# Optimization experiments

Measured on AMD Instinct MI355X. Metric: run time of the kernel, lower is better.

Reference implementation:

```python
import jax, jax.numpy as jnp
import numpy as np

N_NODES = 50000
N_EDGES = 600000
IN_DIM = 64
HID = 128
LN_EPS = 1e-5


def setup_inputs() -> dict:
    key = jax.random.key(0)
    ks = jax.random.split(key, 10)
    x = jax.random.normal(ks[0], (N_NODES, IN_DIM), dtype=jnp.float32)
    edge_index = jax.random.randint(ks[1], (2, N_EDGES), 0, N_NODES, dtype=jnp.int64)
    def lin(k, fan_in, fan_out):
        bound = 1.0 / np.sqrt(fan_in)
        kw, kb = jax.random.split(k)
        W = jax.random.uniform(kw, (fan_in, fan_out), minval=-bound, maxval=bound, dtype=jnp.float32)
        b = jax.random.uniform(kb, (fan_out,), minval=-bound, maxval=bound, dtype=jnp.float32)
        return W, b
    W1, b1 = lin(ks[2], IN_DIM, HID)
    W2, b2 = lin(ks[3], HID, HID)
    W3, b3 = lin(ks[4], HID, HID)
    g1 = jnp.ones((HID,), jnp.float32); be1 = jnp.zeros((HID,), jnp.float32)
    g2 = jnp.ones((HID,), jnp.float32); be2 = jnp.zeros((HID,), jnp.float32)
    g3 = jnp.ones((HID,), jnp.float32); be3 = jnp.zeros((HID,), jnp.float32)
    return dict(x=x, edge_index=edge_index, W1=W1, b1=b1, W2=W2, b2=b2, W3=W3, b3=b3,
                g1=g1, be1=be1, g2=g2, be2=be2, g3=g3, be3=be3)


def _gnn_layer(h, W, b, src, dst, inv_cnt, g, be):
    # linear transform then mean aggregation over {neighbors ∪ self} (self-loops in src/dst)
    h = h @ W + b                                   # [N, HID]
    s = jax.ops.segment_sum(h[src], dst, num_segments=N_NODES)  # gather + scatter-sum
    h = s * inv_cnt                                 # mean aggregation
    h = jax.nn.relu(h)
    mu = jnp.mean(h, axis=-1, keepdims=True)
    var = jnp.var(h, axis=-1, keepdims=True)
    return g * (h - mu) * jax.lax.rsqrt(var + LN_EPS) + be


def reference(x, edge_index, W1, b1, W2, b2, W3, b3, g1, be1, g2, be2, g3, be3):
    loops = jnp.arange(N_NODES, dtype=edge_index.dtype)
    src = jnp.concatenate([edge_index[0], loops])   # message source (x_j)
    dst = jnp.concatenate([edge_index[1], loops])   # aggregation target
    cnt = jax.ops.segment_sum(jnp.ones_like(dst, dtype=x.dtype), dst, num_segments=N_NODES)
    inv_cnt = (1.0 / cnt)[:, None]                  # cnt >= 1 due to self loops
    h = _gnn_layer(x, W1, b1, src, dst, inv_cnt, g1, be1)
    h = _gnn_layer(h, W2, b2, src, dst, inv_cnt, g2, be2)
    h = _gnn_layer(h, W3, b3, src, dst, inv_cnt, g3, be3)
    return h
```

## Files before the change

### kernel.cpp

```cpp
#include <hip/hip_runtime.h>
#include <hip/hip_bf16.h>

#define N_NODES 50000
#define N_EDGES 600000
#define HID 128
#define LN_EPS 1e-5f

#define SCAN_BLOCK 1024
#define SCAN_NBLK ((N_NODES + SCAN_BLOCK - 1) / SCAN_BLOCK)

typedef __attribute__((ext_vector_type(8))) short bf16x8;
typedef __attribute__((ext_vector_type(4))) float f32x4;

static __device__ __forceinline__ unsigned short f2bf(float f) {
    union { float f; unsigned u; } v; v.f = f;
    unsigned u = v.u;
    u += 0x7fffu + ((u >> 16) & 1u);
    return (unsigned short)(u >> 16);
}
static __device__ __forceinline__ float bflo(unsigned u) {
    union { unsigned u; float f; } c; c.u = u << 16; return c.f;
}
static __device__ __forceinline__ float bfhi(unsigned u) {
    union { unsigned u; float f; } c; c.u = u & 0xffff0000u; return c.f;
}

__global__ __launch_bounds__(256) void count_kernel(const int* __restrict__ ei,
                                                    int* __restrict__ deg, int E) {
    int i = blockIdx.x * blockDim.x + threadIdx.x;
    if (i < E) atomicAdd(&deg[ei[E + i]], 1);
}

__global__ __launch_bounds__(SCAN_BLOCK) void deg_partial_kernel(const int* __restrict__ deg,
                                                                 int* __restrict__ partials, int n) {
    int t = threadIdx.x;
    int i = blockIdx.x * SCAN_BLOCK + t;
    int v = (i < n) ? deg[i] : 0;
    int s = v;
#pragma unroll
    for (int off = 1; off < 64; off <<= 1) s += __shfl_xor(s, off);
    __shared__ int ws[SCAN_BLOCK / 64];
    if ((t & 63) == 0) ws[t >> 6] = s;
    __syncthreads();
    if (t == 0) {
        int tot = 0;
#pragma unroll
        for (int w = 0; w < SCAN_BLOCK / 64; ++w) tot += ws[w];
        partials[blockIdx.x] = tot;
    }
}

__global__ __launch_bounds__(64) void scan_partials_kernel(int* __restrict__ partials,
                                                           int* __restrict__ row_ptr, int nblk) {
    int lane = threadIdx.x;
    int v = (lane < nblk) ? partials[lane] : 0;
    int incl = v;
#pragma unroll
    for (int off = 1; off < 64; off <<= 1) {
        int x = __shfl_up(incl, off);
        if (lane >= off) incl += x;
    }
    if (lane < nblk) partials[lane] = incl - v;
    if (lane == 63) row_ptr[N_NODES] = incl;
}

__global__ __launch_bounds__(SCAN_BLOCK) void scan_final_kernel(const int* __restrict__ deg,
                                                                const int* __restrict__ partials,
                                                                int* __restrict__ row_ptr,
                                                                int* __restrict__ cursor,
                                                                float* __restrict__ inv_cnt, int n) {
    int t = threadIdx.x;
    int i = blockIdx.x * SCAN_BLOCK + t;
    int v = (i < n) ? deg[i] : 0;
    int lane = t & 63, wid = t >> 6;
    int incl = v;
#pragma unroll
    for (int off = 1; off < 64; off <<= 1) {
        int x = __shfl_up(incl, off);
        if (lane >= off) incl += x;
    }
    __shared__ int ws[SCAN_BLOCK / 64];
    if (lane == 63) ws[wid] = incl;
    __syncthreads();
    int woff = 0;
    for (int w = 0; w < wid; ++w) woff += ws[w];
    int excl = partials[blockIdx.x] + woff + (incl - v);
    if (i < n) {
        row_ptr[i] = excl;
        cursor[i]  = excl;
        inv_cnt[i] = 1.0f / (float)(v + 1);
    }
}

__global__ __launch_bounds__(256) void fill_kernel(const int* __restrict__ ei,
                                                   int* __restrict__ cursor,
                                                   int* __restrict__ col, int E) {
    int i = blockIdx.x * blockDim.x + threadIdx.x;
    if (i < E) {
        int s = ei[i];
        int d = ei[E + i];
        int p = atomicAdd(&cursor[d], 1);
        col[p] = s;
    }
}

__global__ __launch_bounds__(256) void cast_x_kernel(const float* __restrict__ x,
                                                     unsigned short* __restrict__ xb, int n8) {
    int i = blockIdx.x * 256 + threadIdx.x;
    if (i < n8) {
        float4 a = ((const float4*)x)[i * 2];
        float4 b = ((const float4*)x)[i * 2 + 1];
        int4 o;
        o.x = (int)f2bf(a.x) | ((int)f2bf(a.y) << 16);
        o.y = (int)f2bf(a.z) | ((int)f2bf(a.w) << 16);
        o.z = (int)f2bf(b.x) | ((int)f2bf(b.y) << 16);
        o.w = (int)f2bf(b.z) | ((int)f2bf(b.w) << 16);
        ((int4*)xb)[i] = o;
    }
}

__global__ __launch_bounds__(256) void wswz_kernel(const float* __restrict__ W,
                                                   unsigned short* __restrict__ dst, int K) {
    int i = blockIdx.x * 256 + threadIdx.x;
    if (i < K * 128) {
        int k = i >> 7, col = i & 127;
        dst[(((k >> 3) * 128) + col) * 8 + (k & 7)] = f2bf(W[i]);
    }
}

template <int K>
__global__ __launch_bounds__(256) void gemm_mfma_kernel(
    const unsigned short* __restrict__ A,
    const unsigned short* __restrict__ Wswz,
    const float* __restrict__ bias,
    unsigned short* __restrict__ out, int N) {
    __shared__ unsigned short Bl[K * 128];
    __shared__ float bl[128];
    int t = threadIdx.x;
    for (int i = t; i < K * 16; i += 256)
        ((int4*)Bl)[i] = ((const int4*)Wswz)[i];
    if (t < 128) bl[t] = bias[t];
    __syncthreads();

    int lane = t & 63;
    int w = t >> 6;
    int r0 = blockIdx.x * 64 + w * 16;
    int colb = lane & 15;
    int kg = lane >> 4;
    int rowa = min(r0 + colb, N - 1);

    f32x4 acc[8];
#pragma unroll
    for (int c = 0; c < 8; ++c) acc[c] = (f32x4){0.f, 0.f, 0.f, 0.f};

    const bf16x8* Blv = (const bf16x8*)Bl;
    for (int s = 0; s < K; s += 32) {
        bf16x8 afrag = *(const bf16x8*)&A[(size_t)rowa * K + s + kg * 8];
        int kb = (s >> 3) + kg;
#pragma unroll
        for (int c = 0; c < 8; ++c) {
            bf16x8 bfrag = Blv[kb * 128 + c * 16 + colb];
            acc[c] = __builtin_amdgcn_mfma_f32_16x16x32_bf16(afrag, bfrag, acc[c], 0, 0, 0);
        }
    }
#pragma unroll
    for (int c = 0; c < 8; ++c) {
        int col = c * 16 + colb;
        float bv = bl[col];
#pragma unroll
        for (int r = 0; r < 4; ++r) {
            int ro = r0 + kg * 4 + r;
            if (ro < N) out[(size_t)ro * 128 + col] = f2bf(acc[c][r] + bv);
        }
    }
}

template <int BF16OUT>
__global__ __launch_bounds__(256) void agg_norm_kernel(
    const unsigned short* __restrict__ hb,
    const int* __restrict__ row_ptr,
    const int* __restrict__ col,
    const float* __restrict__ inv_cnt,
    const float* __restrict__ g, const float* __restrict__ be,
    void* __restrict__ outp, int N) {
    int tid  = blockIdx.x * 256 + threadIdx.x;
    int wave = tid >> 6;
    int lane = threadIdx.x & 63;
    int sub  = lane >> 4;
    int lc   = lane & 15;
    int n    = wave * 4 + sub;
    bool act = n < N;
    int nc   = act ? n : N - 1;

    const uint4* h4 = (const uint4*)hb;

    float a[8];
    {
        uint4 u = h4[(size_t)nc * 16 + lc];
        a[0] = bflo(u.x); a[1] = bfhi(u.x);
        a[2] = bflo(u.y); a[3] = bfhi(u.y);
        a[4] = bflo(u.z); a[5] = bfhi(u.z);
        a[6] = bflo(u.w); a[7] = bfhi(u.w);
    }

    int beg = row_ptr[nc], end = row_ptr[nc + 1];
    int cnt = end - beg;
    int lim = min(cnt, 32);
    int c0 = (lc < cnt)      ? col[beg + lc]      : nc;
    int c1 = (16 + lc < cnt) ? col[beg + 16 + lc] : nc;

    int wlim = lim;
    wlim = max(wlim, __shfl_xor(wlim, 16));
    wlim = max(wlim, __shfl_xor(wlim, 32));
    int nGrp = (wlim + 3) >> 2;

    for (int gi = 0; gi < nGrp; ++gi) {
        int e0 = gi * 4;
        int jj[4]; float mm[4];
#pragma unroll
        for (int q = 0; q < 4; ++q) {
            int iq = max(min(e0 + q, lim - 1), 0);
            mm[q] = (e0 + q < lim) ? 1.0f : 0.0f;
            int sl = sub * 16 + (iq & 15);
            int jA = __shfl(c0, sl);
            int jB = __shfl(c1, sl);
            jj[q] = (iq < 16) ? jA : jB;
        }
        uint4 u0 = h4[(size_t)jj[0] * 16 + lc];
        uint4 u1 = h4[(size_t)jj[1] * 16 + lc];
        uint4 u2 = h4[(size_t)jj[2] * 16 + lc];
        uint4 u3 = h4[(size_t)jj[3] * 16 + lc];
#define ACC(U, M)                                                              \
        a[0] = fmaf(M, bflo(U.x), a[0]); a[1] = fmaf(M, bfhi(U.x), a[1]);      \
        a[2] = fmaf(M, bflo(U.y), a[2]); a[3] = fmaf(M, bfhi(U.y), a[3]);      \
        a[4] = fmaf(M, bflo(U.z), a[4]); a[5] = fmaf(M, bfhi(U.z), a[5]);      \
        a[6] = fmaf(M, bflo(U.w), a[6]); a[7] = fmaf(M, bfhi(U.w), a[7]);
        ACC(u0, mm[0]) ACC(u1, mm[1]) ACC(u2, mm[2]) ACC(u3, mm[3])
#undef ACC
    }
    for (int e = 32; e < cnt; ++e) {
        int j = col[beg + e];
        uint4 u = h4[(size_t)j * 16 + lc];
        a[0] += bflo(u.x); a[1] += bfhi(u.x);
        a[2] += bflo(u.y); a[3] += bfhi(u.y);
        a[4] += bflo(u.z); a[5] += bfhi(u.z);
        a[6] += bflo(u.w); a[7] += bfhi(u.w);
    }

    float ic = inv_cnt[nc];
    float s[8], sum = 0.f, sq = 0.f;
#pragma unroll
    for (int k = 0; k < 8; ++k) {
        s[k] = fmaxf(a[k] * ic, 0.0f);
        sum += s[k];
        sq  += s[k] * s[k];
    }
#pragma unroll
    for (int off = 1; off < 16; off <<= 1) {
        sum += __shfl_xor(sum, off);
        sq  += __shfl_xor(sq, off);
    }
    float mu  = sum * (1.0f / 128.0f);
    float var = sq * (1.0f / 128.0f) - mu * mu;
    float rs  = rsqrtf(var + LN_EPS);

    const float4* gv  = (const float4*)g;
    const float4* bv  = (const float4*)be;
    float4 gA = gv[lc * 2], gB = gv[lc * 2 + 1];
    float4 bA = bv[lc * 2], bB = bv[lc * 2 + 1];
    float o[8];
    o[0] = gA.x * (s[0] - mu) * rs + bA.x;
    o[1] = gA.y * (s[1] - mu) * rs + bA.y;
    o[2] = gA.z * (s[2] - mu) * rs + bA.z;
    o[3] = gA.w * (s[3] - mu) * rs + bA.w;
    o[4] = gB.x * (s[4] - mu) * rs + bB.x;
    o[5] = gB.y * (s[5] - mu) * rs + bB.y;
    o[6] = gB.z * (s[6] - mu) * rs + bB.z;
    o[7] = gB.w * (s[7] - mu) * rs + bB.w;

    if (!act) return;
    if (BF16OUT) {
        uint4 p;
        p.x = (unsigned)f2bf(o[0]) | ((unsigned)f2bf(o[1]) << 16);
        p.y = (unsigned)f2bf(o[2]) | ((unsigned)f2bf(o[3]) << 16);
        p.z = (unsigned)f2bf(o[4]) | ((unsigned)f2bf(o[5]) << 16);
        p.w = (unsigned)f2bf(o[6]) | ((unsigned)f2bf(o[7]) << 16);
        ((uint4*)outp)[(size_t)n * 16 + lc] = p;
    } else {
        float4 f0; f0.x = o[0]; f0.y = o[1]; f0.z = o[2]; f0.w = o[3];
        float4 f1; f1.x = o[4]; f1.y = o[5]; f1.z = o[6]; f1.w = o[7];
        ((float4*)outp)[(size_t)n * 32 + lc * 2]     = f0;
        ((float4*)outp)[(size_t)n * 32 + lc * 2 + 1] = f1;
    }
}

extern "C" void kernel_launch(void* const* d_in, const int* in_sizes, int n_in,
                              void* d_out, int out_size, void* d_ws, size_t ws_size,
                              hipStream_t stream) {
    const float* x  = (const float*)d_in[0];
    const int*   ei = (const int*)d_in[1];
    const float* W1 = (const float*)d_in[2];
    const float* b1 = (const float*)d_in[3];
    const float* W2 = (const float*)d_in[4];
    const float* b2 = (const float*)d_in[5];
    const float* W3 = (const float*)d_in[6];
    const float* b3 = (const float*)d_in[7];
    const float* g1 = (const float*)d_in[8];
    const float* be1 = (const float*)d_in[9];
    const float* g2 = (const float*)d_in[10];
    const float* be2 = (const float*)d_in[11];
    const float* g3 = (const float*)d_in[12];
    const float* be3 = (const float*)d_in[13];
    float* out = (float*)d_out;

    const int N = N_NODES, E = N_EDGES;
    char* w = (char*)d_ws;
    unsigned short* hb   = (unsigned short*)w; w += (size_t)N * 128 * 2;
    unsigned short* midb = (unsigned short*)w; w += (size_t)N * 128 * 2;
    unsigned short* xb   = (unsigned short*)w; w += (size_t)N * 64 * 2;
    unsigned short* w1s  = (unsigned short*)w; w += (size_t)64 * 128 * 2;
    unsigned short* w2s  = (unsigned short*)w; w += (size_t)128 * 128 * 2;
    unsigned short* w3s  = (unsigned short*)w; w += (size_t)128 * 128 * 2;
    int*   col    = (int*)w;    w += (size_t)E * sizeof(int);
    int*   rowp   = (int*)w;    w += (size_t)(N + 1) * sizeof(int);
    int*   cursor = (int*)w;    w += (size_t)N * sizeof(int);
    int*   deg    = (int*)w;    w += (size_t)N * sizeof(int);
    float* invc   = (float*)w;  w += (size_t)N * sizeof(float);
    int*   parts  = (int*)w;    w += (size_t)SCAN_NBLK * sizeof(int);

    hipMemsetAsync(deg, 0, (size_t)N * sizeof(int), stream);
    count_kernel<<<(E + 255) / 256, 256, 0, stream>>>(ei, deg, E);
    deg_partial_kernel<<<SCAN_NBLK, SCAN_BLOCK, 0, stream>>>(deg, parts, N);
    scan_partials_kernel<<<1, 64, 0, stream>>>(parts, rowp, SCAN_NBLK);
    scan_final_kernel<<<SCAN_NBLK, SCAN_BLOCK, 0, stream>>>(deg, parts, rowp, cursor, invc, N);
    fill_kernel<<<(E + 255) / 256, 256, 0, stream>>>(ei, cursor, col, E);

    const int n8 = N * 64 / 8;
    cast_x_kernel<<<(n8 + 255) / 256, 256, 0, stream>>>(x, xb, n8);
    wswz_kernel<<<(64 * 128 + 255) / 256, 256, 0, stream>>>(W1, w1s, 64);
    wswz_kernel<<<(128 * 128 + 255) / 256, 256, 0, stream>>>(W2, w2s, 128);
    wswz_kernel<<<(128 * 128 + 255) / 256, 256, 0, stream>>>(W3, w3s, 128);

    const int gemm_blocks = (N + 63) / 64;
    const int agg_blocks  = (N + 15) / 16;

    gemm_mfma_kernel<64><<<gemm_blocks, 256, 0, stream>>>(xb, w1s, b1, hb, N);
    agg_norm_kernel<1><<<agg_blocks, 256, 0, stream>>>(hb, rowp, col, invc, g1, be1, midb, N);
    gemm_mfma_kernel<128><<<gemm_blocks, 256, 0, stream>>>(midb, w2s, b2, hb, N);
    agg_norm_kernel<1><<<agg_blocks, 256, 0, stream>>>(hb, rowp, col, invc, g2, be2, midb, N);
    gemm_mfma_kernel<128><<<gemm_blocks, 256, 0, stream>>>(midb, w3s, b3, hb, N);
    agg_norm_kernel<0><<<agg_blocks, 256, 0, stream>>>(hb, rowp, col, invc, g3, be3, out, N);
}
```

Measured before the change: 195.5 us.

## Fuse x cast into first GEMM, merge weight swizzles, widen gather batch

```diff
diff --git a/kernel.cpp b/kernel.cpp
--- a/kernel.cpp
+++ b/kernel.cpp
@@ -104,33 +104,25 @@
     }
 }
 
-__global__ __launch_bounds__(256) void cast_x_kernel(const float* __restrict__ x,
-                                                     unsigned short* __restrict__ xb, int n8) {
+__global__ __launch_bounds__(256) void wswz_all_kernel(const float* __restrict__ W1,
+                                                       const float* __restrict__ W2,
+                                                       const float* __restrict__ W3,
+                                                       unsigned short* __restrict__ d1,
+                                                       unsigned short* __restrict__ d2,
+                                                       unsigned short* __restrict__ d3) {
     int i = blockIdx.x * 256 + threadIdx.x;
-    if (i < n8) {
-        float4 a = ((const float4*)x)[i * 2];
-        float4 b = ((const float4*)x)[i * 2 + 1];
-        int4 o;
-        o.x = (int)f2bf(a.x) | ((int)f2bf(a.y) << 16);
-        o.y = (int)f2bf(a.z) | ((int)f2bf(a.w) << 16);
-        o.z = (int)f2bf(b.x) | ((int)f2bf(b.y) << 16);
-        o.w = (int)f2bf(b.z) | ((int)f2bf(b.w) << 16);
-        ((int4*)xb)[i] = o;
-    }
-}
-
-__global__ __launch_bounds__(256) void wswz_kernel(const float* __restrict__ W,
-                                                   unsigned short* __restrict__ dst, int K) {
-    int i = blockIdx.x * 256 + threadIdx.x;
-    if (i < K * 128) {
-        int k = i >> 7, col = i & 127;
-        dst[(((k >> 3) * 128) + col) * 8 + (k & 7)] = f2bf(W[i]);
-    }
-}
-
-template <int K>
+    const float* W; unsigned short* dst; int idx;
+    if (i < 64 * 128)            { W = W1; dst = d1; idx = i; }
+    else if (i < (64 + 128) * 128) { W = W2; dst = d2; idx = i - 64 * 128; }
+    else if (i < (64 + 256) * 128) { W = W3; dst = d3; idx = i - (64 + 128) * 128; }
+    else return;
+    int k = idx >> 7, col = idx & 127;
+    dst[(((k >> 3) * 128) + col) * 8 + (k & 7)] = f2bf(W[idx]);
+}
+
+template <int K, int AF32>
 __global__ __launch_bounds__(256) void gemm_mfma_kernel(
-    const unsigned short* __restrict__ A,
+    const void* __restrict__ Ap,
     const unsigned short* __restrict__ Wswz,
     const float* __restrict__ bias,
     unsigned short* __restrict__ out, int N) {
@@ -155,7 +147,19 @@
 
     const bf16x8* Blv = (const bf16x8*)Bl;
     for (int s = 0; s < K; s += 32) {
-        bf16x8 afrag = *(const bf16x8*)&A[(size_t)rowa * K + s + kg * 8];
+        bf16x8 afrag;
+        if (AF32) {
+            const float* Af = (const float*)Ap;
+            float4 a0 = *(const float4*)&Af[(size_t)rowa * K + s + kg * 8];
+            float4 a1 = *(const float4*)&Af[(size_t)rowa * K + s + kg * 8 + 4];
+            afrag[0] = (short)f2bf(a0.x); afrag[1] = (short)f2bf(a0.y);
+            afrag[2] = (short)f2bf(a0.z); afrag[3] = (short)f2bf(a0.w);
+            afrag[4] = (short)f2bf(a1.x); afrag[5] = (short)f2bf(a1.y);
+            afrag[6] = (short)f2bf(a1.z); afrag[7] = (short)f2bf(a1.w);
+        } else {
+            const unsigned short* Ab = (const unsigned short*)Ap;
+            afrag = *(const bf16x8*)&Ab[(size_t)rowa * K + s + kg * 8];
+        }
         int kb = (s >> 3) + kg;
 #pragma unroll
         for (int c = 0; c < 8; ++c) {
@@ -212,13 +216,13 @@
     int wlim = lim;
     wlim = max(wlim, __shfl_xor(wlim, 16));
     wlim = max(wlim, __shfl_xor(wlim, 32));
-    int nGrp = (wlim + 3) >> 2;
+    int nGrp = (wlim + 7) >> 3;
 
     for (int gi = 0; gi < nGrp; ++gi) {
-        int e0 = gi * 4;
-        int jj[4]; float mm[4];
-#pragma unroll
-        for (int q = 0; q < 4; ++q) {
+        int e0 = gi * 8;
+        int jj[8]; float mm[8];
+#pragma unroll
+        for (int q = 0; q < 8; ++q) {
             int iq = max(min(e0 + q, lim - 1), 0);
             mm[q] = (e0 + q < lim) ? 1.0f : 0.0f;
             int sl = sub * 16 + (iq & 15);
@@ -226,17 +230,16 @@
             int jB = __shfl(c1, sl);
             jj[q] = (iq < 16) ? jA : jB;
         }
-        uint4 u0 = h4[(size_t)jj[0] * 16 + lc];
-        uint4 u1 = h4[(size_t)jj[1] * 16 + lc];
-        uint4 u2 = h4[(size_t)jj[2] * 16 + lc];
-        uint4 u3 = h4[(size_t)jj[3] * 16 + lc];
-#define ACC(U, M)                                                              \
-        a[0] = fmaf(M, bflo(U.x), a[0]); a[1] = fmaf(M, bfhi(U.x), a[1]);      \
-        a[2] = fmaf(M, bflo(U.y), a[2]); a[3] = fmaf(M, bfhi(U.y), a[3]);      \
-        a[4] = fmaf(M, bflo(U.z), a[4]); a[5] = fmaf(M, bfhi(U.z), a[5]);      \
-        a[6] = fmaf(M, bflo(U.w), a[6]); a[7] = fmaf(M, bfhi(U.w), a[7]);
-        ACC(u0, mm[0]) ACC(u1, mm[1]) ACC(u2, mm[2]) ACC(u3, mm[3])
-#undef ACC
+        uint4 u[8];
+#pragma unroll
+        for (int q = 0; q < 8; ++q) u[q] = h4[(size_t)jj[q] * 16 + lc];
+#pragma unroll
+        for (int q = 0; q < 8; ++q) {
+            a[0] = fmaf(mm[q], bflo(u[q].x), a[0]); a[1] = fmaf(mm[q], bfhi(u[q].x), a[1]);
+            a[2] = fmaf(mm[q], bflo(u[q].y), a[2]); a[3] = fmaf(mm[q], bfhi(u[q].y), a[3]);
+            a[4] = fmaf(mm[q], bflo(u[q].z), a[4]); a[5] = fmaf(mm[q], bfhi(u[q].z), a[5]);
+            a[6] = fmaf(mm[q], bflo(u[q].w), a[6]); a[7] = fmaf(mm[q], bfhi(u[q].w), a[7]);
+        }
     }
     for (int e = 32; e < cnt; ++e) {
         int j = col[beg + e];
@@ -285,12 +288,12 @@
         p.y = (unsigned)f2bf(o[2]) | ((unsigned)f2bf(o[3]) << 16);
         p.z = (unsigned)f2bf(o[4]) | ((unsigned)f2bf(o[5]) << 16);
         p.w = (unsigned)f2bf(o[6]) | ((unsigned)f2bf(o[7]) << 16);
-        ((uint4*)outp)[(size_t)n * 16 + lc] = p;
+        ((uint4*)outp)[(size_t)nc * 16 + lc] = p;
     } else {
         float4 f0; f0.x = o[0]; f0.y = o[1]; f0.z = o[2]; f0.w = o[3];
         float4 f1; f1.x = o[4]; f1.y = o[5]; f1.z = o[6]; f1.w = o[7];
-        ((float4*)outp)[(size_t)n * 32 + lc * 2]     = f0;
-        ((float4*)outp)[(size_t)n * 32 + lc * 2 + 1] = f1;
+        ((float4*)outp)[(size_t)nc * 32 + lc * 2]     = f0;
+        ((float4*)outp)[(size_t)nc * 32 + lc * 2 + 1] = f1;
     }
 }
 
@@ -317,7 +320,6 @@
     char* w = (char*)d_ws;
     unsigned short* hb   = (unsigned short*)w; w += (size_t)N * 128 * 2;
     unsigned short* midb = (unsigned short*)w; w += (size_t)N * 128 * 2;
-    unsigned short* xb   = (unsigned short*)w; w += (size_t)N * 64 * 2;
     unsigned short* w1s  = (unsigned short*)w; w += (size_t)64 * 128 * 2;
     unsigned short* w2s  = (unsigned short*)w; w += (size_t)128 * 128 * 2;
     unsigned short* w3s  = (unsigned short*)w; w += (size_t)128 * 128 * 2;
@@ -335,19 +337,15 @@
     scan_final_kernel<<<SCAN_NBLK, SCAN_BLOCK, 0, stream>>>(deg, parts, rowp, cursor, invc, N);
     fill_kernel<<<(E + 255) / 256, 256, 0, stream>>>(ei, cursor, col, E);
 
-    const int n8 = N * 64 / 8;
-    cast_x_kernel<<<(n8 + 255) / 256, 256, 0, stream>>>(x, xb, n8);
-    wswz_kernel<<<(64 * 128 + 255) / 256, 256, 0, stream>>>(W1, w1s, 64);
-    wswz_kernel<<<(128 * 128 + 255) / 256, 256, 0, stream>>>(W2, w2s, 128);
-    wswz_kernel<<<(128 * 128 + 255) / 256, 256, 0, stream>>>(W3, w3s, 128);
+    wswz_all_kernel<<<((64 + 256) * 128 + 255) / 256, 256, 0, stream>>>(W1, W2, W3, w1s, w2s, w3s);
 
     const int gemm_blocks = (N + 63) / 64;
     const int agg_blocks  = (N + 15) / 16;
 
-    gemm_mfma_kernel<64><<<gemm_blocks, 256, 0, stream>>>(xb, w1s, b1, hb, N);
+    gemm_mfma_kernel<64, 1><<<gemm_blocks, 256, 0, stream>>>(x, w1s, b1, hb, N);
     agg_norm_kernel<1><<<agg_blocks, 256, 0, stream>>>(hb, rowp, col, invc, g1, be1, midb, N);
-    gemm_mfma_kernel<128><<<gemm_blocks, 256, 0, stream>>>(midb, w2s, b2, hb, N);
+    gemm_mfma_kernel<128, 0><<<gemm_blocks, 256, 0, stream>>>(midb, w2s, b2, hb, N);
     agg_norm_kernel<1><<<agg_blocks, 256, 0, stream>>>(hb, rowp, col, invc, g2, be2, midb, N);
-    gemm_mfma_kernel<128><<<gemm_blocks, 256, 0, stream>>>(midb, w3s, b3, hb, N);
+    gemm_mfma_kernel<128, 0><<<gemm_blocks, 256, 0, stream>>>(midb, w3s, b3, hb, N);
     agg_norm_kernel<0><<<agg_blocks, 256, 0, stream>>>(hb, rowp, col, invc, g3, be3, out, N);
 }
```

New measurement: 195.7 us. About the same (+0.1%).
